# Kernel tuning notes

Measured on AMD Instinct MI355X. Metric: run time of the kernel, lower is better.

## Reference

```python
import jax, jax.numpy as jnp
import numpy as np

B, S, H, NH = 4, 1024, 1024, 16
HD = H // NH
CAUSAL_HEADS = 4
META_HEADS = NH // 4
CAUSAL_W = 0.7                      # cognitive_state['reasoning']['causal_active'] > 0.5 -> branch on
META_W = ((0.9 - 0.8) / 0.2) * 0.3  # awareness_level = 0.9 > 0.8 -> meta branch on, blend = 0.15


def _mha(xq, xkv, Win, bi, Wout, bout, nh):
    """torch nn.MultiheadAttention (batch_first) with packed in_proj [H, 3H]."""
    b, sq, h = xq.shape
    sk = xkv.shape[1]
    hd = h // nh
    q = (xq @ Win[:, :h] + bi[:h]).reshape(b, sq, nh, hd).transpose(0, 2, 1, 3)
    k = (xkv @ Win[:, h:2 * h] + bi[h:2 * h]).reshape(b, sk, nh, hd).transpose(0, 2, 1, 3)
    v = (xkv @ Win[:, 2 * h:] + bi[2 * h:]).reshape(b, sk, nh, hd).transpose(0, 2, 1, 3)
    scores = jnp.einsum('bhqd,bhkd->bhqk', q, k) / jnp.sqrt(jnp.asarray(hd, q.dtype))
    probs = jax.nn.softmax(scores, axis=-1)
    ctx = jnp.einsum('bhqk,bhkd->bhqd', probs, v)
    return ctx.transpose(0, 2, 1, 3).reshape(b, sq, h) @ Wout + bout


def _forward(hidden_states, cons_vec, Wq, bq, Wk, bk, Wv, bv, cg_W, cg_b, am_W, am_b,
             ca_Win, ca_bin, ca_Wout, ca_bout, mc_Win, mc_bin, mc_Wout, mc_bout, Wo, bo):
    b, s, h = hidden_states.shape
    q = (hidden_states @ Wq + bq).reshape(b, s, NH, HD).transpose(0, 2, 1, 3)
    k = (hidden_states @ Wk + bk).reshape(b, s, NH, HD).transpose(0, 2, 1, 3)
    v = (hidden_states @ Wv + bv).reshape(b, s, NH, HD).transpose(0, 2, 1, 3)
    scores = jnp.einsum('bhqd,bhkd->bhqk', q, k) / jnp.sqrt(jnp.asarray(HD, q.dtype))
    # consciousness-gated score modulation: sigmoid(gate(x) + awareness(cons_vec)) per (query, head)
    mod = jax.nn.sigmoid(hidden_states @ cg_W + cg_b + (cons_vec @ am_W + am_b))  # [B,S,NH]
    scores = scores * mod.transpose(0, 2, 1)[..., None]  # [B,NH,S,1] broadcast over keys
    probs = jax.nn.softmax(scores, axis=-1)
    ctx = jnp.einsum('bhqk,bhkd->bhqd', probs, v).transpose(0, 2, 1, 3).reshape(b, s, h)
    # causal MHA branch (active: causal_active=0.7 > 0.5)
    causal_ctx = _mha(hidden_states, hidden_states, ca_Win, ca_bin, ca_Wout, ca_bout, CAUSAL_HEADS)
    ctx = ctx * (1.0 - CAUSAL_W) + causal_ctx * CAUSAL_W
    # metacognitive MHA branch (active: awareness=0.9 > 0.8)
    meta_ctx = _mha(ctx, ctx, mc_Win, mc_bin, mc_Wout, mc_bout, META_HEADS)
    ctx = ctx * (1.0 - META_W) + meta_ctx * META_W
    return ctx @ Wo + bo


def setup_inputs() -> dict:
    key = jax.random.key(0)
    ks = jax.random.split(key, 16)
    sc = 0.02
    d = {
        'hidden_states': jax.random.normal(ks[0], (B, S, H), jnp.float32),
        'cons_vec': jax.random.uniform(ks[1], (16,), jnp.float32),
        'Wq': jax.random.normal(ks[2], (H, H), jnp.float32) * sc, 'bq': jnp.zeros((H,), jnp.float32),
        'Wk': jax.random.normal(ks[3], (H, H), jnp.float32) * sc, 'bk': jnp.zeros((H,), jnp.float32),
        'Wv': jax.random.normal(ks[4], (H, H), jnp.float32) * sc, 'bv': jnp.zeros((H,), jnp.float32),
        'cg_W': jax.random.normal(ks[5], (H, NH), jnp.float32) * sc, 'cg_b': jnp.zeros((NH,), jnp.float32),
        'am_W': jax.random.normal(ks[6], (16, NH), jnp.float32) * sc, 'am_b': jnp.zeros((NH,), jnp.float32),
        'ca_Win': jax.random.normal(ks[7], (H, 3 * H), jnp.float32) * sc, 'ca_bin': jnp.zeros((3 * H,), jnp.float32),
        'ca_Wout': jax.random.normal(ks[8], (H, H), jnp.float32) * sc, 'ca_bout': jnp.zeros((H,), jnp.float32),
        'mc_Win': jax.random.normal(ks[9], (H, 3 * H), jnp.float32) * sc, 'mc_bin': jnp.zeros((3 * H,), jnp.float32),
        'mc_Wout': jax.random.normal(ks[10], (H, H), jnp.float32) * sc, 'mc_bout': jnp.zeros((H,), jnp.float32),
        'Wo': jax.random.normal(ks[11], (H, H), jnp.float32) * sc, 'bo': jnp.zeros((H,), jnp.float32),
    }
    return d


def reference(hidden_states, cons_vec, Wq, bq, Wk, bk, Wv, bv, cg_W, cg_b, am_W, am_b,
              ca_Win, ca_bin, ca_Wout, ca_bout, mc_Win, mc_bin, mc_Wout, mc_bout, Wo, bo):
    return _forward(hidden_states, cons_vec, Wq, bq, Wk, bk, Wv, bv, cg_W, cg_b, am_W, am_b,
                    ca_Win, ca_bin, ca_Wout, ca_bout, mc_Win, mc_bin, mc_Wout, mc_bout, Wo, bo)
```

## Files before the change

kernel.cpp:

```cpp
#include <hip/hip_runtime.h>
#include <stdint.h>

typedef unsigned short u16;
typedef __attribute__((ext_vector_type(8))) short short8;
typedef __attribute__((ext_vector_type(4))) float f32x4;
typedef __attribute__((ext_vector_type(16))) float f32x16;

#define MFMA16(a,b,c) __builtin_amdgcn_mfma_f32_16x16x32_bf16((a),(b),(c),0,0,0)
#define MFMA32(a,b,c) __builtin_amdgcn_mfma_f32_32x32x16_bf16((a),(b),(c),0,0,0)

__device__ __forceinline__ float fast_exp2(float x) {
  return __builtin_amdgcn_exp2f(x);
}

__device__ __forceinline__ u16 f2bf(float f) {
  union { float f; uint32_t u; } v; v.f = f;
  uint32_t r = v.u + 0x7FFFu + ((v.u >> 16) & 1u);
  return (u16)(r >> 16);
}
__device__ __forceinline__ float bf2f(uint32_t u) {
  union { uint32_t i; float f; } v; v.i = u << 16; return v.f;
}
__device__ __forceinline__ uint32_t pack_bf16_rne(float lo, float hi) {
  return (uint32_t)f2bf(lo) | ((uint32_t)f2bf(hi) << 16);
}
__device__ __forceinline__ void async_copy16(void* lds, const void* g) {
  __builtin_amdgcn_global_load_lds(
      (const __attribute__((address_space(1))) uint32_t*)g,
      (__attribute__((address_space(3))) uint32_t*)lds, 16, 0, 0);
}

__device__ __forceinline__ void transpose8x8(uint32_t r[4], int lane8) {
  uint32_t a0, a1, a2, a3;
  a0 = __shfl_xor(r[0], 4); a1 = __shfl_xor(r[1], 4);
  a2 = __shfl_xor(r[2], 4); a3 = __shfl_xor(r[3], 4);
  if (lane8 & 4) { r[0] = a2; r[1] = a3; } else { r[2] = a0; r[3] = a1; }
  a0 = __shfl_xor(r[0], 2); a1 = __shfl_xor(r[1], 2);
  a2 = __shfl_xor(r[2], 2); a3 = __shfl_xor(r[3], 2);
  if (lane8 & 2) { r[0] = a1; r[2] = a3; } else { r[1] = a0; r[3] = a2; }
  a0 = __shfl_xor(r[0], 1); a1 = __shfl_xor(r[1], 1);
  a2 = __shfl_xor(r[2], 1); a3 = __shfl_xor(r[3], 1);
  uint32_t sel = (lane8 & 1) ? 0x03020706u : 0x05040100u;
  r[0] = __builtin_amdgcn_perm(a0, r[0], sel);
  r[1] = __builtin_amdgcn_perm(a1, r[1], sel);
  r[2] = __builtin_amdgcn_perm(a2, r[2], sel);
  r[3] = __builtin_amdgcn_perm(a3, r[3], sel);
}

__global__ __launch_bounds__(256) void castmod_kernel(
    const float* __restrict__ X, u16* __restrict__ Xbf,
    const float* __restrict__ cgW, const float* __restrict__ cgb,
    const float* __restrict__ cons, const float* __restrict__ amW,
    const float* __restrict__ amb, float* __restrict__ modp) {
  __shared__ float xs[1024];
  __shared__ float part[16][16];
  __shared__ float am[16];
  int row = blockIdx.x, t = threadIdx.x;
  {
    float4 v = ((const float4*)(X + (size_t)row * 1024))[t];
    xs[t * 4 + 0] = v.x; xs[t * 4 + 1] = v.y; xs[t * 4 + 2] = v.z; xs[t * 4 + 3] = v.w;
    uint2 o;
    o.x = (uint32_t)f2bf(v.x) | ((uint32_t)f2bf(v.y) << 16);
    o.y = (uint32_t)f2bf(v.z) | ((uint32_t)f2bf(v.w) << 16);
    ((uint2*)Xbf)[(size_t)row * 256 + t] = o;
  }
  if (t < 16) {
    float a = amb[t];
#pragma unroll
    for (int i = 0; i < 16; i++) a += cons[i] * amW[i * 16 + t];
    am[t] = a;
  }
  __syncthreads();
  int h = t & 15, ch = t >> 4;
  float p = 0.f;
#pragma unroll 8
  for (int k = ch * 64; k < ch * 64 + 64; k++) p += xs[k] * cgW[k * 16 + h];
  part[ch][h] = p;
  __syncthreads();
  if (t < 16) {
    float s = cgb[t] + am[t];
#pragma unroll
    for (int c = 0; c < 16; c++) s += part[c][t];
    int b = row >> 10, si = row & 1023;
    modp[((size_t)(b * 16 + t)) * 1024 + si] = 0.18033688f / (1.f + __expf(-s));
  }
}

struct PrepArgs {
  const float* src[12];
  u16* dst[12];
  int sstride[12];
  const float* cabin; const float* bq; const float* bk; const float* bv;
  float* biasBig; float* lbuf;
};
__global__ __launch_bounds__(256) void prep_weights(PrepArgs p) {
  int z = blockIdx.z;
  int tx = threadIdx.x & 31, ty = threadIdx.x >> 5;
  if (z < 12) {
    __shared__ float tile[32][33];
    const float* __restrict__ in = p.src[z];
    u16* __restrict__ out = p.dst[z];
    int sstr = p.sstride[z];
    int c0 = blockIdx.x * 32, r0 = blockIdx.y * 32;
#pragma unroll
    for (int j = 0; j < 4; j++)
      tile[ty + j * 8][tx] = in[(size_t)(r0 + ty + j * 8) * sstr + c0 + tx];
    __syncthreads();
#pragma unroll
    for (int j = 0; j < 4; j++)
      out[(size_t)(c0 + ty + j * 8) * 1024 + r0 + tx] = f2bf(tile[tx][ty + j * 8]);
  } else {
    int id = blockIdx.y * 32 + blockIdx.x, t = threadIdx.x;
    if (id < 24) {
      int i = id * 256 + t;
      float v;
      if (i < 3072) v = p.cabin[i];
      else if (i < 4096) v = p.bq[i - 3072];
      else if (i < 5120) v = p.bk[i - 4096];
      else v = p.bv[i - 5120];
      p.biasBig[i] = v;
    } else if (id < 152) {
      p.lbuf[(id - 24) * 256 + t] = 0.f;
    }
  }
}

template <int OUT_F32, int HAS_EXTRA, int BN>
__global__ __launch_bounds__(256, 4) void gemm_bt(
    const u16* __restrict__ A, const u16* __restrict__ Bt,
    const float* __restrict__ bias, const u16* __restrict__ extra,
    float alpha, float beta, void* __restrict__ Cout, int M, int N, int K) {
  constexpr int NJ = BN / 32;
  __shared__ u16 As[128 * 64];
  __shared__ u16 Bs[BN * 64];
  const int t = threadIdx.x;
  const int w = t >> 6, l = t & 63, lm = l & 15, lg = l >> 4;
  const int wm = w & 1, wn = w >> 1;
  const int m0 = blockIdx.y * 128, n0 = blockIdx.x * BN;
  const int rl = l >> 3, gsrc8 = ((l & 7) ^ (rl & 7)) * 8;
  const f32x4 fzero = {0.f, 0.f, 0.f, 0.f};
  f32x4 acc[4][NJ];
#pragma unroll
  for (int i = 0; i < 4; i++)
#pragma unroll
    for (int j = 0; j < NJ; j++) acc[i][j] = fzero;

  for (int kt = 0; kt < K; kt += 64) {
    __syncthreads();
#pragma unroll
    for (int c = 0; c < 4; c++) {
      int rb = c * 32 + w * 8;
      async_copy16(&As[rb * 64], A + (size_t)(m0 + rb + rl) * K + kt + gsrc8);
    }
#pragma unroll
    for (int c = 0; c < BN / 32; c++) {
      int rb = c * 32 + w * 8;
      async_copy16(&Bs[rb * 64], Bt + (size_t)(n0 + rb + rl) * K + kt + gsrc8);
    }
    __syncthreads();
#pragma unroll
    for (int kk = 0; kk < 2; kk++) {
      short8 af[4], bf[NJ];
      const int gph = ((kk * 4 + lg) ^ (lm & 7)) * 8;
#pragma unroll
      for (int i = 0; i < 4; i++)
        af[i] = *(const short8*)&As[(wm * 64 + i * 16 + lm) * 64 + gph];
#pragma unroll
      for (int j = 0; j < NJ; j++)
        bf[j] = *(const short8*)&Bs[(wn * (BN / 2) + j * 16 + lm) * 64 + gph];
#pragma unroll
      for (int i = 0; i < 4; i++)
#pragma unroll
        for (int j = 0; j < NJ; j++) acc[i][j] = MFMA16(af[i], bf[j], acc[i][j]);
    }
  }
#pragma unroll
  for (int i = 0; i < 4; i++) {
    int row0 = m0 + wm * 64 + i * 16 + lg * 4;
#pragma unroll
    for (int j = 0; j < NJ; j++) {
      int col = n0 + wn * (BN / 2) + j * 16 + lm;
      float bc = bias[col];
#pragma unroll
      for (int r = 0; r < 4; r++) {
        size_t idx = (size_t)(row0 + r) * N + col;
        float v = acc[i][j][r] + bc;
        if constexpr (HAS_EXTRA) v = alpha * v + beta * bf2f(extra[idx]);
        if constexpr (OUT_F32) ((float*)Cout)[idx] = v;
        else ((u16*)Cout)[idx] = f2bf(v);
      }
    }
  }
}

__global__ __launch_bounds__(256, 4) void gemm_in3(
    const u16* __restrict__ A, const u16* __restrict__ BtBig,
    const float* __restrict__ bias, u16* __restrict__ qkOut,
    u16* __restrict__ Vtb, u16* __restrict__ qkvm) {
  constexpr int K = 1024;
  __shared__ u16 As[128 * 64];
  __shared__ u16 Bs[128 * 64];
  const int t = threadIdx.x;
  const int w = t >> 6, l = t & 63, lm = l & 15, lg = l >> 4;
  const int wm = w & 1, wn = w >> 1;
  const int m0 = blockIdx.y * 128, n0 = blockIdx.x * 128;
  const int rl = l >> 3, gsrc8 = ((l & 7) ^ (rl & 7)) * 8;
  const f32x4 fzero = {0.f, 0.f, 0.f, 0.f};
  f32x4 acc[4][4];
#pragma unroll
  for (int i = 0; i < 4; i++)
#pragma unroll
    for (int j = 0; j < 4; j++) acc[i][j] = fzero;

  for (int kt = 0; kt < K; kt += 64) {
    __syncthreads();
#pragma unroll
    for (int c = 0; c < 4; c++) {
      int rb = c * 32 + w * 8;
      async_copy16(&As[rb * 64], A + (size_t)(m0 + rb + rl) * K + kt + gsrc8);
      async_copy16(&Bs[rb * 64], BtBig + (size_t)(n0 + rb + rl) * K + kt + gsrc8);
    }
    __syncthreads();
#pragma unroll
    for (int kk = 0; kk < 2; kk++) {
      short8 af[4], bf[4];
      const int gph = ((kk * 4 + lg) ^ (lm & 7)) * 8;
#pragma unroll
      for (int i = 0; i < 4; i++)
        af[i] = *(const short8*)&As[(wm * 64 + i * 16 + lm) * 64 + gph];
#pragma unroll
      for (int j = 0; j < 4; j++)
        bf[j] = *(const short8*)&Bs[(wn * 64 + j * 16 + lm) * 64 + gph];
#pragma unroll
      for (int i = 0; i < 4; i++)
#pragma unroll
        for (int j = 0; j < 4; j++) acc[i][j] = MFMA16(af[i], bf[j], acc[i][j]);
    }
  }
#pragma unroll
  for (int i = 0; i < 4; i++) {
    int row0 = m0 + wm * 64 + i * 16 + lg * 4;
#pragma unroll
    for (int j = 0; j < 4; j++) {
      int col = n0 + wn * 64 + j * 16 + lm;
      float bc = bias[col];
      if (col < 2048) {
#pragma unroll
        for (int r = 0; r < 4; r++)
          qkOut[(size_t)(row0 + r) * 2048 + col] = f2bf(acc[i][j][r] + bc);
      } else if (col < 3072) {
        int b = row0 >> 10, q0 = row0 & 1023;
        int z = b * 4 + ((col - 2048) >> 8), d = (col - 2048) & 255;
        union { u16 pk[4]; uint2 v; } u;
#pragma unroll
        for (int r = 0; r < 4; r++) u.pk[r] = f2bf(acc[i][j][r] + bc);
        *(uint2*)&Vtb[((size_t)z * 256 + d) * 1024 + q0] = u.v;
      } else {
#pragma unroll
        for (int r = 0; r < 4; r++)
          qkvm[(size_t)(row0 + r) * 3072 + col - 3072] = f2bf(acc[i][j][r] + bc);
      }
    }
  }
}

__device__ __forceinline__ void qk_body(
    char* smem, const u16* __restrict__ qk, u16* __restrict__ P,
    float* __restrict__ lrow, float scale2, int nb, int mb, int z) {
  constexpr int QKS = 2048;
  u16* As = (u16*)smem;
  u16* Bs = (u16*)(smem + 128 * 64 * 2);
  const int t = threadIdx.x;
  const int w = t >> 6, l = t & 63, lm = l & 15, lg = l >> 4;
  const int wm = w & 1, wn = w >> 1;
  const int b = z >> 2, h = z & 3;
  const int m0 = mb * 128, n0 = nb * 128;
  const u16* Abase = qk + ((size_t)b << 10) * QKS + h * 256;
  const u16* Bbase = qk + ((size_t)b << 10) * QKS + 1024 + h * 256;
  const int rl = l >> 3, gsrc8 = ((l & 7) ^ (rl & 7)) * 8;
  const f32x4 fzero = {0.f, 0.f, 0.f, 0.f};
  f32x4 acc[4][4];
#pragma unroll
  for (int i = 0; i < 4; i++)
#pragma unroll
    for (int j = 0; j < 4; j++) acc[i][j] = fzero;

#pragma unroll
  for (int kt = 0; kt < 256; kt += 64) {
    __syncthreads();
#pragma unroll
    for (int c = 0; c < 4; c++) {
      int rb = c * 32 + w * 8;
      async_copy16(&As[rb * 64], Abase + (size_t)(m0 + rb + rl) * QKS + kt + gsrc8);
      async_copy16(&Bs[rb * 64], Bbase + (size_t)(n0 + rb + rl) * QKS + kt + gsrc8);
    }
    __syncthreads();
#pragma unroll
    for (int kk = 0; kk < 2; kk++) {
      short8 af[4], bf[4];
      const int gph = ((kk * 4 + lg) ^ (lm & 7)) * 8;
#pragma unroll
      for (int i = 0; i < 4; i++)
        af[i] = *(const short8*)&As[(wm * 64 + i * 16 + lm) * 64 + gph];
#pragma unroll
      for (int j = 0; j < 4; j++)
        bf[j] = *(const short8*)&Bs[(wn * 64 + j * 16 + lm) * 64 + gph];
#pragma unroll
      for (int i = 0; i < 4; i++)
#pragma unroll
        for (int j = 0; j < 4; j++) acc[i][j] = MFMA16(af[i], bf[j], acc[i][j]);
    }
  }
  u16* Pz = P + ((size_t)z << 20);
#pragma unroll
  for (int i = 0; i < 4; i++) {
    int row0 = m0 + wm * 64 + i * 16 + lg * 4;
    float rsum[4] = {0.f, 0.f, 0.f, 0.f};
#pragma unroll
    for (int j = 0; j < 4; j++) {
      int col = n0 + wn * 64 + j * 16 + lm;
#pragma unroll
      for (int r = 0; r < 4; r++) {
        float p = fast_exp2(acc[i][j][r] * scale2);
        rsum[r] += p;
        Pz[(size_t)(row0 + r) * 1024 + col] = f2bf(p);
      }
    }
#pragma unroll
    for (int r = 0; r < 4; r++) {
      float s = rsum[r];
#pragma unroll
      for (int sh = 1; sh <= 8; sh <<= 1) s += __shfl_xor(s, sh);
      if (lm == 0) atomicAdd(&lrow[(z << 10) + row0 + r], s);
    }
  }
}

__global__ __launch_bounds__(256, 4) void gemm_qk_exp(
    const u16* __restrict__ qk, u16* __restrict__ P, float* __restrict__ lrow,
    float scale2) {
  __shared__ char smem[2 * 128 * 64 * 2];
  qk_body(smem, qk, P, lrow, scale2, blockIdx.x, blockIdx.y, blockIdx.z);
}

__device__ __forceinline__ void flash_body(
    char* smem, const u16* __restrict__ qkv, const float* __restrict__ modp,
    u16* __restrict__ outp, int fid) {
  constexpr int S = 1024, W3 = 3072, HD = 64, BKV = 128;
  constexpr int VSTR = 136;
  u16* Ks = (u16*)smem;
  u16* Vt = (u16*)(smem + 16384);

  const int t = threadIdx.x, w = t >> 6, l = t & 63, l31 = l & 31, hl = l >> 5;
  const int rest = fid >> 3;
  const int q0 = (rest & 7) * 128;
  const int bh = (fid & 7) + 8 * (rest >> 3);
  const int b = bh >> 4, h = bh & 15;
  const size_t rowbase = (size_t)b * S;
  const int qw = q0 + w * 32;

  const int oc = t >> 3, kvo = t & 7;
  const int sd0 = (oc & 7) * 8;
  const int skvg = (oc >> 3) * 8;

  short8 qf[4];
  {
    const u16* qp = qkv + (rowbase + qw + l31) * W3 + h * HD + hl * 8;
#pragma unroll
    for (int ks = 0; ks < 4; ks++) qf[ks] = *(const short8*)(qp + ks * 16);
  }
  const float rs = modp[(size_t)bh * S + qw + l31];
  float lsum = 0.f;
  f32x16 oacc[2];
#pragma unroll
  for (int d = 0; d < 2; d++)
#pragma unroll
    for (int i = 0; i < 16; i++) oacc[d][i] = 0.f;

  short8 vpre[4];
#pragma unroll
  for (int c = 0; c < 4; c++) {
    int kv = c * 32 + skvg + kvo;
    vpre[c] = *(const short8*)(qkv + (rowbase + kv) * W3 + 2048 + h * HD + sd0);
  }

  for (int kb = 0; kb < S; kb += BKV) {
    __syncthreads();
#pragma unroll
    for (int c = 0; c < 4; c++) {
      int rb = c * 32 + w * 8;
      int row = rb + (l >> 3);
      int gsrc = ((l & 7) ^ (row & 7)) * 8;
      async_copy16(&Ks[rb * HD],
                   qkv + (rowbase + kb + row) * W3 + 1024 + h * HD + gsrc);
    }
#pragma unroll
    for (int c = 0; c < 4; c++) {
      union { short8 s; uint32_t u[4]; } vv, vo;
      vv.s = vpre[c];
      uint32_t r[4] = {vv.u[0], vv.u[1], vv.u[2], vv.u[3]};
      transpose8x8(r, kvo);
      vo.u[0] = r[0]; vo.u[1] = r[1]; vo.u[2] = r[2]; vo.u[3] = r[3];
      *(short8*)&Vt[(sd0 + kvo) * VSTR + c * 32 + skvg] = vo.s;
    }
    __syncthreads();
    if (kb + BKV < S) {
#pragma unroll
      for (int c = 0; c < 4; c++) {
        int kv = c * 32 + skvg + kvo;
        vpre[c] = *(const short8*)(qkv + (rowbase + kb + BKV + kv) * W3 + 2048 + h * HD + sd0);
      }
    }

    __builtin_amdgcn_s_setprio(1);
#pragma unroll
    for (int n = 0; n < 4; n++) {
      f32x16 st;
#pragma unroll
      for (int i = 0; i < 16; i++) st[i] = 0.f;
      const int krow = n * 32 + l31;
#pragma unroll
      for (int ks = 0; ks < 4; ks++) {
        int g = ks * 2 + hl;
        short8 kf = *(const short8*)&Ks[krow * HD + ((g ^ (krow & 7)) * 8)];
        st = MFMA32(kf, qf[ks], st);
      }
      uint32_t pk8[8];
#pragma unroll
      for (int tt = 0; tt < 4; tt++) {
#pragma unroll
        for (int s = 0; s < 2; s++) {
          float p0 = fast_exp2(st[tt * 4 + 2 * s] * rs);
          float p1 = fast_exp2(st[tt * 4 + 2 * s + 1] * rs);
          lsum += p0 + p1;
          pk8[tt * 2 + s] = pack_bf16_rne(p0, p1);
        }
      }
#pragma unroll
      for (int k2 = 0; k2 < 2; k2++) {
        const int ta = 2 * k2, tb = ta + 1;
        uint32_t pw[4];
#pragma unroll
        for (int s = 0; s < 2; s++) {
          uint32_t A = pk8[ta * 2 + s], B = pk8[tb * 2 + s];
          uint32_t Ax = __shfl_xor(A, 32), Bx = __shfl_xor(B, 32);
          pw[s] = hl ? Bx : A;
          pw[2 + s] = hl ? B : Ax;
        }
        union { uint32_t u[4]; short8 s8; } pt;
        pt.u[0] = pw[0]; pt.u[1] = pw[1]; pt.u[2] = pw[2]; pt.u[3] = pw[3];
        const int ks = 2 * n + k2;
#pragma unroll
        for (int dt = 0; dt < 2; dt++) {
          short8 vb = *(const short8*)&Vt[(dt * 32 + l31) * VSTR + ks * 16 + hl * 8];
          oacc[dt] = MFMA32(vb, pt.s8, oacc[dt]);
        }
      }
    }
    __builtin_amdgcn_s_setprio(0);
  }
  float sfull = lsum + __shfl_xor(lsum, 32);
  const float invl = 1.f / sfull;
#pragma unroll
  for (int dt = 0; dt < 2; dt++) {
#pragma unroll
    for (int tt = 0; tt < 4; tt++) {
      union { u16 pkv[4]; uint2 v; } u;
#pragma unroll
      for (int r = 0; r < 4; r++) u.pkv[r] = f2bf(oacc[dt][tt * 4 + r] * invl);
      *(uint2*)&outp[(rowbase + qw + l31) * 1024 + h * HD + dt * 32 + tt * 8 + hl * 4] = u.v;
    }
  }
}

__global__ __launch_bounds__(256, 4) void fused_qk_flash(
    const u16* __restrict__ qkvm, const float* __restrict__ modp,
    u16* __restrict__ ctxm, const u16* __restrict__ caQK,
    u16* __restrict__ P, float* __restrict__ lrow, float scale2) {
  __shared__ char smem[33792];
  const int bid = blockIdx.x;
  if (bid < 512) {
    flash_body(smem, qkvm, modp, ctxm, bid);
  } else {
    int qid = bid - 512;
    qk_body(smem, caQK, P, lrow, scale2, qid & 7, (qid >> 3) & 7, qid >> 6);
  }
}

__global__ __launch_bounds__(256, 4) void gemm_pv(
    const u16* __restrict__ P, const u16* __restrict__ Vtb,
    const float* __restrict__ lrow, u16* __restrict__ outp) {
  constexpr int K = 1024, BN = 64, NJ = 2;
  __shared__ u16 As[128 * 64];
  __shared__ u16 Bs[BN * 64];
  const int t = threadIdx.x;
  const int w = t >> 6, l = t & 63, lm = l & 15, lg = l >> 4;
  const int wm = w & 1, wn = w >> 1;
  const int z = blockIdx.z, b = z >> 2, h = z & 3;
  const int m0 = blockIdx.y * 128, n0 = blockIdx.x * BN;
  const u16* Abase = P + ((size_t)z << 20);
  const u16* Bbase = Vtb + ((size_t)z << 18);
  const int rl = l >> 3, gsrc8 = ((l & 7) ^ (rl & 7)) * 8;
  const f32x4 fzero = {0.f, 0.f, 0.f, 0.f};
  f32x4 acc[4][NJ];
#pragma unroll
  for (int i = 0; i < 4; i++)
#pragma unroll
    for (int j = 0; j < NJ; j++) acc[i][j] = fzero;

  for (int kt = 0; kt < K; kt += 64) {
    __syncthreads();
#pragma unroll
    for (int c = 0; c < 4; c++) {
      int rb = c * 32 + w * 8;
      async_copy16(&As[rb * 64], Abase + (size_t)(m0 + rb + rl) * K + kt + gsrc8);
    }
#pragma unroll
    for (int c = 0; c < BN / 32; c++) {
      int rb = c * 32 + w * 8;
      async_copy16(&Bs[rb * 64], Bbase + (size_t)(n0 + rb + rl) * K + kt + gsrc8);
    }
    __syncthreads();
#pragma unroll
    for (int kk = 0; kk < 2; kk++) {
      short8 af[4], bf[NJ];
      const int gph = ((kk * 4 + lg) ^ (lm & 7)) * 8;
#pragma unroll
      for (int i = 0; i < 4; i++)
        af[i] = *(const short8*)&As[(wm * 64 + i * 16 + lm) * 64 + gph];
#pragma unroll
      for (int j = 0; j < NJ; j++)
        bf[j] = *(const short8*)&Bs[(wn * (BN / 2) + j * 16 + lm) * 64 + gph];
#pragma unroll
      for (int i = 0; i < 4; i++)
#pragma unroll
        for (int j = 0; j < NJ; j++) acc[i][j] = MFMA16(af[i], bf[j], acc[i][j]);
    }
  }
#pragma unroll
  for (int i = 0; i < 4; i++) {
    int row0 = m0 + wm * 64 + i * 16 + lg * 4;
    float invl[4];
#pragma unroll
    for (int r = 0; r < 4; r++) invl[r] = 1.f / lrow[(z << 10) + row0 + r];
#pragma unroll
    for (int j = 0; j < NJ; j++) {
      int col = n0 + wn * (BN / 2) + j * 16 + lm;
#pragma unroll
      for (int r = 0; r < 4; r++)
        outp[(size_t)((b << 10) + row0 + r) * 1024 + h * 256 + col] =
            f2bf(acc[i][j][r] * invl[r]);
    }
  }
}

extern "C" void kernel_launch(void* const* d_in, const int* in_sizes, int n_in,
                              void* d_out, int out_size, void* d_ws, size_t ws_size,
                              hipStream_t stream) {
  (void)in_sizes; (void)n_in; (void)out_size; (void)ws_size;
  const float* X      = (const float*)d_in[0];
  const float* cons   = (const float*)d_in[1];
  const float* Wq     = (const float*)d_in[2];  const float* bq     = (const float*)d_in[3];
  const float* Wk     = (const float*)d_in[4];  const float* bk     = (const float*)d_in[5];
  const float* Wv     = (const float*)d_in[6];  const float* bv     = (const float*)d_in[7];
  const float* cgW    = (const float*)d_in[8];  const float* cgb    = (const float*)d_in[9];
  const float* amW    = (const float*)d_in[10]; const float* amb    = (const float*)d_in[11];
  const float* caWin  = (const float*)d_in[12]; const float* cabin  = (const float*)d_in[13];
  const float* caWout = (const float*)d_in[14]; const float* cabout = (const float*)d_in[15];
  const float* mcWin  = (const float*)d_in[16]; const float* mcbin  = (const float*)d_in[17];
  const float* mcWout = (const float*)d_in[18]; const float* mcbout = (const float*)d_in[19];
  const float* Wo     = (const float*)d_in[20]; const float* bo     = (const float*)d_in[21];

  char* ws = (char*)d_ws;
  size_t off = 0;
  auto alloc = [&](size_t bytes) -> void* {
    void* p = ws + off; off += (bytes + 255) & ~(size_t)255; return p;
  };
  u16*    Xbf     = (u16*)alloc((size_t)4096 * 1024 * 2);
  u16*    BtBig   = (u16*)alloc((size_t)6144 * 1024 * 2);
  u16*    mcWinT  = (u16*)alloc((size_t)3072 * 1024 * 2);
  u16*    caWoutT = (u16*)alloc((size_t)1024 * 1024 * 2);
  u16*    mcWoutT = (u16*)alloc((size_t)1024 * 1024 * 2);
  u16*    WoT     = (u16*)alloc((size_t)1024 * 1024 * 2);
  float*  biasBig = (float*)alloc(6144 * 4);
  float*  modb    = (float*)alloc((size_t)64 * 1024 * 4);
  u16*    caQK    = (u16*)alloc((size_t)4096 * 2048 * 2);
  u16*    qkvm    = (u16*)alloc((size_t)4096 * 3072 * 2);
  u16*    actx    = (u16*)alloc((size_t)4096 * 1024 * 2);
  u16*    ctxm    = (u16*)alloc((size_t)4096 * 1024 * 2);
  u16*    ctx1    = (u16*)alloc((size_t)4096 * 1024 * 2);
  u16*    Pbuf    = (u16*)alloc((size_t)16 * 1024 * 1024 * 2);
  u16*    Vtb     = (u16*)alloc((size_t)16 * 256 * 1024 * 2);
  float*  lbuf    = (float*)alloc((size_t)2 * 16384 * 4);
  float*  l_ca    = lbuf;
  float*  l_mc    = lbuf + 16384;
  u16*    mcQK    = caQK;
  u16*    mctx    = ctxm;
  u16*    ctx2    = actx;

  const float SC2 = 1.4426950408889634f / 16.f;

  castmod_kernel<<<4096, 256, 0, stream>>>(X, Xbf, cgW, cgb, cons, amW, amb, modb);
  {
    PrepArgs pa;
    for (int s = 0; s < 3; s++) {
      pa.src[s] = caWin + s * 1024; pa.dst[s] = BtBig + (size_t)s * 1024 * 1024;
      pa.sstride[s] = 3072;
    }
    pa.src[3] = Wq; pa.dst[3] = BtBig + (size_t)3072 * 1024; pa.sstride[3] = 1024;
    pa.src[4] = Wk; pa.dst[4] = BtBig + (size_t)4096 * 1024; pa.sstride[4] = 1024;
    pa.src[5] = Wv; pa.dst[5] = BtBig + (size_t)5120 * 1024; pa.sstride[5] = 1024;
    for (int s = 0; s < 3; s++) {
      pa.src[6 + s] = mcWin + s * 1024; pa.dst[6 + s] = mcWinT + (size_t)s * 1024 * 1024;
      pa.sstride[6 + s] = 3072;
    }
    pa.src[9]  = caWout; pa.dst[9]  = caWoutT; pa.sstride[9]  = 1024;
    pa.src[10] = mcWout; pa.dst[10] = mcWoutT; pa.sstride[10] = 1024;
    pa.src[11] = Wo;     pa.dst[11] = WoT;     pa.sstride[11] = 1024;
    pa.cabin = cabin; pa.bq = bq; pa.bk = bk; pa.bv = bv;
    pa.biasBig = biasBig; pa.lbuf = lbuf;
    prep_weights<<<dim3(32, 32, 13), 256, 0, stream>>>(pa);
  }

  gemm_in3<<<dim3(48, 32), 256, 0, stream>>>(Xbf, BtBig, biasBig, caQK, Vtb, qkvm);
  fused_qk_flash<<<1536, 256, 0, stream>>>(qkvm, modb, ctxm, caQK, Pbuf, l_ca, SC2);
  gemm_pv<<<dim3(4, 8, 16), 256, 0, stream>>>(Pbuf, Vtb, l_ca, actx);
  gemm_bt<0, 1, 64><<<dim3(16, 32), 256, 0, stream>>>(actx, caWoutT, cabout, ctxm, 0.7f, 0.3f,
                                                      ctx1, 4096, 1024, 1024);
  gemm_in3<<<dim3(24, 32), 256, 0, stream>>>(ctx1, mcWinT, mcbin, mcQK, Vtb, qkvm );
  gemm_qk_exp<<<dim3(8, 8, 16), 256, 0, stream>>>(mcQK, Pbuf, l_mc, SC2);
  gemm_pv<<<dim3(4, 8, 16), 256, 0, stream>>>(Pbuf, Vtb, l_mc, mctx);
  gemm_bt<0, 1, 64><<<dim3(16, 32), 256, 0, stream>>>(mctx, mcWoutT, mcbout, ctx1, 0.15f, 0.85f,
                                                      ctx2, 4096, 1024, 1024);
  gemm_bt<1, 0, 64><<<dim3(16, 32), 256, 0, stream>>>(ctx2, WoT, bo, nullptr, 0.f, 0.f,
                                                      d_out, 4096, 1024, 1024);
}
```

Before: 415.7 us.

## Double-buffer LDS tiles in gemm_bt and gemm_pv to overlap loads with MFMA

Converts the generic bt GEMM and the P·V GEMM from single-buffered shared-memory tiles to a two-stage ping-pong pipeline. The next K-tile is prefetched asynchronously while MFMAs run on the current one, which removes one barrier per iteration. This doubles LDS use per block, so the launch-bounds occupancy hint drops from 4 to 3. The hint for gemm_in3 also rises to 5. Correctness depends on the async copy having landed by the trailing barrier, and the lower occupancy may offset the gain.

After: 496.1 us. 1.19x slower.

```diff
diff --git a/kernel.cpp b/kernel.cpp
--- a/kernel.cpp
+++ b/kernel.cpp
@@ -126,13 +126,13 @@
 }
 
 template <int OUT_F32, int HAS_EXTRA, int BN>
-__global__ __launch_bounds__(256, 4) void gemm_bt(
+__global__ __launch_bounds__(256, 3) void gemm_bt(
     const u16* __restrict__ A, const u16* __restrict__ Bt,
     const float* __restrict__ bias, const u16* __restrict__ extra,
     float alpha, float beta, void* __restrict__ Cout, int M, int N, int K) {
   constexpr int NJ = BN / 32;
-  __shared__ u16 As[128 * 64];
-  __shared__ u16 Bs[BN * 64];
+  __shared__ u16 As[2][128 * 64];
+  __shared__ u16 Bs[2][BN * 64];
   const int t = threadIdx.x;
   const int w = t >> 6, l = t & 63, lm = l & 15, lg = l >> 4;
   const int wm = w & 1, wn = w >> 1;
@@ -145,34 +145,50 @@
 #pragma unroll
     for (int j = 0; j < NJ; j++) acc[i][j] = fzero;
 
+#pragma unroll
+  for (int c = 0; c < 4; c++) {
+    int rb = c * 32 + w * 8;
+    async_copy16(&As[0][rb * 64], A + (size_t)(m0 + rb + rl) * K + gsrc8);
+  }
+#pragma unroll
+  for (int c = 0; c < BN / 32; c++) {
+    int rb = c * 32 + w * 8;
+    async_copy16(&Bs[0][rb * 64], Bt + (size_t)(n0 + rb + rl) * K + gsrc8);
+  }
+  __syncthreads();
+
+  int cur = 0;
   for (int kt = 0; kt < K; kt += 64) {
-    __syncthreads();
-#pragma unroll
-    for (int c = 0; c < 4; c++) {
-      int rb = c * 32 + w * 8;
-      async_copy16(&As[rb * 64], A + (size_t)(m0 + rb + rl) * K + kt + gsrc8);
-    }
-#pragma unroll
-    for (int c = 0; c < BN / 32; c++) {
-      int rb = c * 32 + w * 8;
-      async_copy16(&Bs[rb * 64], Bt + (size_t)(n0 + rb + rl) * K + kt + gsrc8);
-    }
-    __syncthreads();
+    if (kt + 64 < K) {
+      const int nxt = cur ^ 1;
+#pragma unroll
+      for (int c = 0; c < 4; c++) {
+        int rb = c * 32 + w * 8;
+        async_copy16(&As[nxt][rb * 64], A + (size_t)(m0 + rb + rl) * K + kt + 64 + gsrc8);
+      }
+#pragma unroll
+      for (int c = 0; c < BN / 32; c++) {
+        int rb = c * 32 + w * 8;
+        async_copy16(&Bs[nxt][rb * 64], Bt + (size_t)(n0 + rb + rl) * K + kt + 64 + gsrc8);
+      }
+    }
 #pragma unroll
     for (int kk = 0; kk < 2; kk++) {
       short8 af[4], bf[NJ];
       const int gph = ((kk * 4 + lg) ^ (lm & 7)) * 8;
 #pragma unroll
       for (int i = 0; i < 4; i++)
-        af[i] = *(const short8*)&As[(wm * 64 + i * 16 + lm) * 64 + gph];
+        af[i] = *(const short8*)&As[cur][(wm * 64 + i * 16 + lm) * 64 + gph];
 #pragma unroll
       for (int j = 0; j < NJ; j++)
-        bf[j] = *(const short8*)&Bs[(wn * (BN / 2) + j * 16 + lm) * 64 + gph];
+        bf[j] = *(const short8*)&Bs[cur][(wn * (BN / 2) + j * 16 + lm) * 64 + gph];
 #pragma unroll
       for (int i = 0; i < 4; i++)
 #pragma unroll
         for (int j = 0; j < NJ; j++) acc[i][j] = MFMA16(af[i], bf[j], acc[i][j]);
     }
+    __syncthreads();
+    cur ^= 1;
   }
 #pragma unroll
   for (int i = 0; i < 4; i++) {
@@ -193,7 +209,7 @@
   }
 }
 
-__global__ __launch_bounds__(256, 4) void gemm_in3(
+__global__ __launch_bounds__(256, 5) void gemm_in3(
     const u16* __restrict__ A, const u16* __restrict__ BtBig,
     const float* __restrict__ bias, u16* __restrict__ qkOut,
     u16* __restrict__ Vtb, u16* __restrict__ qkvm) {
@@ -487,12 +503,12 @@
   }
 }
 
-__global__ __launch_bounds__(256, 4) void gemm_pv(
+__global__ __launch_bounds__(256, 3) void gemm_pv(
     const u16* __restrict__ P, const u16* __restrict__ Vtb,
     const float* __restrict__ lrow, u16* __restrict__ outp) {
   constexpr int K = 1024, BN = 64, NJ = 2;
-  __shared__ u16 As[128 * 64];
-  __shared__ u16 Bs[BN * 64];
+  __shared__ u16 As[2][128 * 64];
+  __shared__ u16 Bs[2][BN * 64];
   const int t = threadIdx.x;
   const int w = t >> 6, l = t & 63, lm = l & 15, lg = l >> 4;
   const int wm = w & 1, wn = w >> 1;
@@ -508,34 +524,50 @@
 #pragma unroll
     for (int j = 0; j < NJ; j++) acc[i][j] = fzero;
 
+#pragma unroll
+  for (int c = 0; c < 4; c++) {
+    int rb = c * 32 + w * 8;
+    async_copy16(&As[0][rb * 64], Abase + (size_t)(m0 + rb + rl) * K + gsrc8);
+  }
+#pragma unroll
+  for (int c = 0; c < BN / 32; c++) {
+    int rb = c * 32 + w * 8;
+    async_copy16(&Bs[0][rb * 64], Bbase + (size_t)(n0 + rb + rl) * K + gsrc8);
+  }
+  __syncthreads();
+
+  int cur = 0;
   for (int kt = 0; kt < K; kt += 64) {
-    __syncthreads();
-#pragma unroll
-    for (int c = 0; c < 4; c++) {
-      int rb = c * 32 + w * 8;
-      async_copy16(&As[rb * 64], Abase + (size_t)(m0 + rb + rl) * K + kt + gsrc8);
-    }
-#pragma unroll
-    for (int c = 0; c < BN / 32; c++) {
-      int rb = c * 32 + w * 8;
-      async_copy16(&Bs[rb * 64], Bbase + (size_t)(n0 + rb + rl) * K + kt + gsrc8);
-    }
-    __syncthreads();
+    if (kt + 64 < K) {
+      const int nxt = cur ^ 1;
+#pragma unroll
+      for (int c = 0; c < 4; c++) {
+        int rb = c * 32 + w * 8;
+        async_copy16(&As[nxt][rb * 64], Abase + (size_t)(m0 + rb + rl) * K + kt + 64 + gsrc8);
+      }
+#pragma unroll
+      for (int c = 0; c < BN / 32; c++) {
+        int rb = c * 32 + w * 8;
+        async_copy16(&Bs[nxt][rb * 64], Bbase + (size_t)(n0 + rb + rl) * K + kt + 64 + gsrc8);
+      }
+    }
 #pragma unroll
     for (int kk = 0; kk < 2; kk++) {
       short8 af[4], bf[NJ];
       const int gph = ((kk * 4 + lg) ^ (lm & 7)) * 8;
 #pragma unroll
       for (int i = 0; i < 4; i++)
-        af[i] = *(const short8*)&As[(wm * 64 + i * 16 + lm) * 64 + gph];
+        af[i] = *(const short8*)&As[cur][(wm * 64 + i * 16 + lm) * 64 + gph];
 #pragma unroll
       for (int j = 0; j < NJ; j++)
-        bf[j] = *(const short8*)&Bs[(wn * (BN / 2) + j * 16 + lm) * 64 + gph];
+        bf[j] = *(const short8*)&Bs[cur][(wn * (BN / 2) + j * 16 + lm) * 64 + gph];
 #pragma unroll
       for (int i = 0; i < 4; i++)
 #pragma unroll
         for (int j = 0; j < NJ; j++) acc[i][j] = MFMA16(af[i], bf[j], acc[i][j]);
     }
+    __syncthreads();
+    cur ^= 1;
   }
 #pragma unroll
   for (int i = 0; i < 4; i++) {
```
